# Kernel tuning notes

Measured on AMD Instinct MI355X. Metric: run time of the kernel, lower is better.

## Reference

```python
import jax, jax.numpy as jnp
import numpy as np

GAMMA = 0.2
P = 3
N = 16384


def setup_inputs() -> dict:
    key = jax.random.key(0)
    k1, k2 = jax.random.split(key)
    y_pred = jax.random.normal(k1, (N, 2), dtype=jnp.float32)
    y_true = jax.random.randint(k2, (N,), 0, 2, dtype=jnp.int32)
    return {"y_pred": y_pred, "y_true": y_true}


def reference(y_pred, y_true):
    # softmax over classes, take probability of class 1 -> [N]
    s = jax.nn.softmax(y_pred, axis=-1)[:, 1]
    pos_mask = (y_true == 1)
    neg_mask = ~pos_mask
    # difference[j, i] = pos_i - neg_j - gamma  (rows: negatives, cols: positives)
    diff = s[None, :] - s[:, None] - GAMMA  # [N, N]
    pair = neg_mask[:, None] & pos_mask[None, :]
    valid = pair & (diff < 0.0)
    # sum of (-diff)^p over masked entries == hinge^p penalty
    contrib = jnp.where(valid, (-diff) ** P, jnp.zeros_like(diff))
    return jnp.sum(contrib)
```

## Files before the change

### kernel.cpp

```cpp
#include <hip/hip_runtime.h>
#include <math.h>

#define GAMMA_F 0.2f
#define K1_BS 1024
#define NT 1024
#define NB 512
#define NH (8 * NB)
#define DLO 0.25f
#define DSCALE (NB / 1.5f)
#define SCALE 1.099511627776e12
#define INV_SCALE (1.0 / 1.099511627776e12)

__device__ __forceinline__ float sig2(float2 y) {
    return 1.0f / (1.0f + __expf(y.x - y.y));
}

__device__ __forceinline__ int bucket_of(float x) {
    int k = (int)floorf((x + DLO) * DSCALE);
    return k < 0 ? 0 : (k >= NB ? NB - 1 : k);
}

extern "C" __global__ __launch_bounds__(K1_BS) void k1_hist(
        const float* __restrict__ y_pred, const int* __restrict__ y_true,
        int n, unsigned long long* __restrict__ part) {
    __shared__ unsigned long long H[NH];
    int tid = threadIdx.x;
    for (int i = tid; i < NH; i += K1_BS) H[i] = 0ULL;
    __syncthreads();

    int i = blockIdx.x * K1_BS + tid;
    if (i < n) {
        float2 y = ((const float2*)y_pred)[i];
        float s = sig2(y);
        bool isp = (y_true[i] == 1);
        float x = isp ? s - GAMMA_F : s;
        int off0 = (isp ? 0 : 4 * NB) + bucket_of(x);
        double d = (double)x, d2 = d * d;
        atomicAdd(&H[off0],          (unsigned long long)(long long)SCALE);
        atomicAdd(&H[off0 + NB],     (unsigned long long)(long long)(d * SCALE));
        atomicAdd(&H[off0 + 2 * NB], (unsigned long long)(long long)(d2 * SCALE));
        atomicAdd(&H[off0 + 3 * NB], (unsigned long long)(long long)(d2 * d * SCALE));
    }
    __syncthreads();

    unsigned long long* dst = part + (size_t)blockIdx.x * NH;
    for (int j = tid; j < NH; j += K1_BS) dst[j] = H[j];
}

extern "C" __global__ __launch_bounds__(NT) void k2_reduce(
        int nblk, const unsigned long long* __restrict__ part,
        float* __restrict__ out) {
    __shared__ double H[NH];
    __shared__ double4 wtot[NT / 64];
    __shared__ double wred[NT / 64];

    int tid = threadIdx.x, lane = tid & 63, w = tid >> 6;

    for (int i = tid; i < NH; i += NT) {
        unsigned long long s = 0ULL;
        #pragma unroll 4
        for (int b = 0; b < nblk; ++b) s += part[(size_t)b * NH + i];
        H[i] = (double)(long long)s * INV_SCALE;
    }
    __syncthreads();

    int k = (NB - 1) - tid;
    double c0 = 0.0, c1 = 0.0, c2 = 0.0, c3 = 0.0;
    if (tid < NB) {
        c0 = H[4 * NB + k];
        c1 = H[5 * NB + k];
        c2 = H[6 * NB + k];
        c3 = H[7 * NB + k];
    }
    double i0 = c0, i1 = c1, i2 = c2, i3 = c3;
    #pragma unroll
    for (int d = 1; d < 64; d <<= 1) {
        double t0 = __shfl_up(i0, d, 64);
        double t1 = __shfl_up(i1, d, 64);
        double t2 = __shfl_up(i2, d, 64);
        double t3 = __shfl_up(i3, d, 64);
        if (lane >= d) { i0 += t0; i1 += t1; i2 += t2; i3 += t3; }
    }
    if (lane == 63) wtot[w] = make_double4(i0, i1, i2, i3);
    __syncthreads();

    double term = 0.0;
    if (tid < NB) {
        double o0 = 0.0, o1 = 0.0, o2 = 0.0, o3 = 0.0;
        for (int ww = 0; ww < w; ++ww) {
            double4 t = wtot[ww];
            o0 += t.x; o1 += t.y; o2 += t.z; o3 += t.w;
        }
        double e0 = o0 + i0 - c0;
        double e1 = o1 + i1 - c1;
        double e2 = o2 + i2 - c2;
        double e3 = o3 + i3 - c3;
        double P0 = H[k], P1 = H[NB + k], P2 = H[2 * NB + k], P3 = H[3 * NB + k];
        term = e3 * P0 - 3.0 * e2 * P1 + 3.0 * e1 * P2 - e0 * P3;
    }

    #pragma unroll
    for (int off = 32; off > 0; off >>= 1) term += __shfl_down(term, off, 64);
    if (lane == 0) wred[w] = term;
    __syncthreads();
    if (tid == 0) {
        double t = 0.0;
        #pragma unroll
        for (int ww = 0; ww < NT / 64; ++ww) t += wred[ww];
        out[0] = (float)t;
    }
}

extern "C" void kernel_launch(void* const* d_in, const int* in_sizes, int n_in,
                              void* d_out, int out_size, void* d_ws, size_t ws_size,
                              hipStream_t stream) {
    const float* y_pred = (const float*)d_in[0];
    const int* y_true = (const int*)d_in[1];
    int n = in_sizes[1];
    float* out = (float*)d_out;
    (void)n_in; (void)out_size; (void)ws_size;

    int nblk = (n + K1_BS - 1) / K1_BS;
    unsigned long long* part = (unsigned long long*)d_ws;

    k1_hist<<<dim3(nblk), dim3(K1_BS), 0, stream>>>(y_pred, y_true, n, part);
    k2_reduce<<<dim3(1), dim3(NT), 0, stream>>>(nblk, part, out);
}
```

Before: 68.10 us.

## Fuse histogram and reduction into one kernel using a last-block-done pattern

The two kernels become one. Each block accumulates its histogram bins directly into a global histogram with 64-bit atomics, replacing the per-block shared histogram and its partial copies. A global done counter picks the last finishing block, which reads the global histogram and runs the prefix-scan reduction. This removes the second launch and the pass over per-block partials. In exchange it adds global atomic contention on hot buckets. Correctness also depends on the workspace histogram, counter and reference base being zero or consistent on each call, since nothing resets them.

```diff
diff --git a/kernel.cpp b/kernel.cpp
--- a/kernel.cpp
+++ b/kernel.cpp
@@ -2,8 +2,7 @@
 #include <math.h>
 
 #define GAMMA_F 0.2f
-#define K1_BS 1024
-#define NT 1024
+#define BS 1024
 #define NB 512
 #define NH (8 * NB)
 #define DLO 0.25f
@@ -20,15 +19,22 @@
     return k < 0 ? 0 : (k >= NB ? NB - 1 : k);
 }
 
-extern "C" __global__ __launch_bounds__(K1_BS) void k1_hist(
+extern "C" __global__ __launch_bounds__(BS) void softauc_fused(
         const float* __restrict__ y_pred, const int* __restrict__ y_true,
-        int n, unsigned long long* __restrict__ part) {
-    __shared__ unsigned long long H[NH];
-    int tid = threadIdx.x;
-    for (int i = tid; i < NH; i += K1_BS) H[i] = 0ULL;
-    __syncthreads();
+        int n, int nblk,
+        unsigned long long* __restrict__ hist,
+        unsigned long long* __restrict__ done,
+        const unsigned long long* __restrict__ refbase,
+        float* __restrict__ out) {
+    __shared__ double H[NH];
+    __shared__ double4 wtot[BS / 64];
+    __shared__ double wred[BS / 64];
+    __shared__ int last_flag;
 
-    int i = blockIdx.x * K1_BS + tid;
+    int tid = threadIdx.x, lane = tid & 63, w = tid >> 6;
+    unsigned long long base = *refbase;
+
+    int i = blockIdx.x * BS + tid;
     if (i < n) {
         float2 y = ((const float2*)y_pred)[i];
         float s = sig2(y);
@@ -36,31 +42,24 @@
         float x = isp ? s - GAMMA_F : s;
         int off0 = (isp ? 0 : 4 * NB) + bucket_of(x);
         double d = (double)x, d2 = d * d;
-        atomicAdd(&H[off0],          (unsigned long long)(long long)SCALE);
-        atomicAdd(&H[off0 + NB],     (unsigned long long)(long long)(d * SCALE));
-        atomicAdd(&H[off0 + 2 * NB], (unsigned long long)(long long)(d2 * SCALE));
-        atomicAdd(&H[off0 + 3 * NB], (unsigned long long)(long long)(d2 * d * SCALE));
+        atomicAdd(&hist[off0],          (unsigned long long)(long long)(SCALE));
+        atomicAdd(&hist[off0 + NB],     (unsigned long long)(long long)(d * SCALE));
+        atomicAdd(&hist[off0 + 2 * NB], (unsigned long long)(long long)(d2 * SCALE));
+        atomicAdd(&hist[off0 + 3 * NB], (unsigned long long)(long long)(d2 * d * SCALE));
+    }
+    __threadfence();
+    __syncthreads();
+    if (tid == 0) {
+        unsigned long long old = atomicAdd(done, 1ULL);
+        last_flag = (old - base == (unsigned long long)(nblk - 1)) ? 1 : 0;
     }
     __syncthreads();
+    if (!last_flag) return;
+    __threadfence();
 
-    unsigned long long* dst = part + (size_t)blockIdx.x * NH;
-    for (int j = tid; j < NH; j += K1_BS) dst[j] = H[j];
-}
-
-extern "C" __global__ __launch_bounds__(NT) void k2_reduce(
-        int nblk, const unsigned long long* __restrict__ part,
-        float* __restrict__ out) {
-    __shared__ double H[NH];
-    __shared__ double4 wtot[NT / 64];
-    __shared__ double wred[NT / 64];
-
-    int tid = threadIdx.x, lane = tid & 63, w = tid >> 6;
-
-    for (int i = tid; i < NH; i += NT) {
-        unsigned long long s = 0ULL;
-        #pragma unroll 4
-        for (int b = 0; b < nblk; ++b) s += part[(size_t)b * NH + i];
-        H[i] = (double)(long long)s * INV_SCALE;
+    for (int j = tid; j < NH; j += BS) {
+        unsigned long long v = atomicAdd(&hist[j], 0ULL);
+        H[j] = (double)(long long)(v - base) * INV_SCALE;
     }
     __syncthreads();
 
@@ -106,7 +105,7 @@
     if (tid == 0) {
         double t = 0.0;
         #pragma unroll
-        for (int ww = 0; ww < NT / 64; ++ww) t += wred[ww];
+        for (int ww = 0; ww < BS / 64; ++ww) t += wred[ww];
         out[0] = (float)t;
     }
 }
@@ -120,9 +119,12 @@
     float* out = (float*)d_out;
     (void)n_in; (void)out_size; (void)ws_size;
 
-    int nblk = (n + K1_BS - 1) / K1_BS;
-    unsigned long long* part = (unsigned long long*)d_ws;
+    int nblk = (n + BS - 1) / BS;
+    unsigned long long* W = (unsigned long long*)d_ws;
+    unsigned long long* hist = W;
+    unsigned long long* done = W + NH;
+    unsigned long long* refbase = W + (1 << 17);
 
-    k1_hist<<<dim3(nblk), dim3(K1_BS), 0, stream>>>(y_pred, y_true, n, part);
-    k2_reduce<<<dim3(1), dim3(NT), 0, stream>>>(nblk, part, out);
+    softauc_fused<<<dim3(nblk), dim3(BS), 0, stream>>>(
+        y_pred, y_true, n, nblk, hist, done, refbase, out);
 }
```

Measured after the change: 70.61 us. +3.7%, slower.
